# Kernel tuning notes

Measured on AMD Instinct MI355X. Metric: run time of the kernel, lower is better.

Reference implementation:

```python
import jax, jax.numpy as jnp
import numpy as np
from jax import lax

K_NEI = 64      # max_num_neighbors in radius query
NEG = -1e30     # mask value for max-aggregation


def fps(pos, n_sample):
    """Farthest point sampling per cloud. pos: [B,N,3] -> idx [B,n_sample] int32.
    Deterministic start at point 0 (PyG uses a random start)."""
    B, N, _ = pos.shape
    start = jnp.zeros((B,), jnp.int32)
    big = jnp.full((B, N), jnp.finfo(pos.dtype).max, pos.dtype)
    def body(carry, _):
        mind, last = carry
        lp = jnp.take_along_axis(pos, last[:, None, None], axis=1)  # [B,1,3]
        d = jnp.sum((pos - lp) ** 2, -1)                            # [B,N]
        mind = jnp.minimum(mind, d)
        nxt = jnp.argmax(mind, axis=1).astype(jnp.int32)
        return (mind, nxt), nxt
    (_, _), rest = lax.scan(body, (big, start), None, length=n_sample - 1)
    return jnp.concatenate([start[None], rest], 0).T  # [B, n_sample]


def radius_nn(pos_all, pos_q, r, k):
    """Up to k nearest neighbors within radius r (per cloud).
    pos_all: [B,N,3], pos_q: [B,M,3] -> idx [B,M,k] int32, valid [B,M,k] bool."""
    d2 = jnp.sum((pos_q[:, :, None, :] - pos_all[:, None, :, :]) ** 2, -1)  # [B,M,N]
    score = jnp.where(d2 <= r * r, -d2, -jnp.inf)
    vals, idx = lax.top_k(score, k)
    return idx, jnp.isfinite(vals)


def gather(feat, idx):
    """feat: [B,P,C], idx: [B,M,k] -> [B,M,k,C]"""
    B, M, k = idx.shape
    out = jnp.take_along_axis(feat, idx.reshape(B, M * k)[:, :, None], axis=1)
    return out.reshape(B, M, k, feat.shape[-1])


def mlp3(x, w1, b1, w2, b2, w3, b3):
    x = jax.nn.relu(x @ w1 + b1)
    x = jax.nn.relu(x @ w2 + b2)
    return x @ w3 + b3


def point_conv(x, pos_src, pos_dst, nidx, valid, params):
    """PyG PointConv: message = local_nn([x_j, pos_j - pos_i]), max aggregation."""
    rel = gather(pos_src, nidx) - pos_dst[:, :, None, :]          # [B,M,k,3]
    msg = rel if x is None else jnp.concatenate([gather(x, nidx), rel], -1)
    h = mlp3(msg, *params)                                        # [B,M,k,C]
    h = jnp.where(valid[..., None], h, NEG)
    out = jnp.max(h, axis=2)
    return jnp.where(valid.any(2)[..., None], out, 0.0)


def setup_inputs() -> dict:
    key = jax.random.key(0)
    shapes = {
        'sa1_w1': (3, 64), 'sa1_b1': (64,), 'sa1_w2': (64, 64), 'sa1_b2': (64,),
        'sa1_w3': (64, 128), 'sa1_b3': (128,),
        'sa2_w1': (131, 128), 'sa2_b1': (128,), 'sa2_w2': (128, 128), 'sa2_b2': (128,),
        'sa2_w3': (128, 256), 'sa2_b3': (256,),
        'g_w1': (259, 256), 'g_b1': (256,), 'g_w2': (256, 512), 'g_b2': (512,),
        'g_w3': (512, 1024), 'g_b3': (1024,),
        'l1_w': (1024, 512), 'l1_b': (512,), 'l2_w': (512, 256), 'l2_b': (256,),
        'l3_w': (256, 7), 'l3_b': (7,),
    }
    ks = jax.random.split(key, len(shapes) + 1)
    inp = {'points': jax.random.uniform(ks[0], (8, 4096, 3), jnp.float32)}
    for i, (name, shp) in enumerate(shapes.items()):
        inp[name] = jax.random.normal(ks[i + 1], shp, jnp.float32) / np.sqrt(shp[0]).astype(np.float32)
    return inp


def reference(points, sa1_w1, sa1_b1, sa1_w2, sa1_b2, sa1_w3, sa1_b3,
              sa2_w1, sa2_b1, sa2_w2, sa2_b2, sa2_w3, sa2_b3,
              g_w1, g_b1, g_w2, g_b2, g_w3, g_b3,
              l1_w, l1_b, l2_w, l2_b, l3_w, l3_b):
    B, N, _ = points.shape
    pos = points[..., :3]
    # ---- stage 1: fps ratio 0.5, radius 0.1 ----
    N1 = N // 2
    idx1 = fps(pos, N1)
    pos1 = jnp.take_along_axis(pos, idx1[..., None], axis=1)      # [B,N1,3]
    nidx1, valid1 = radius_nn(pos, pos1, 0.1, K_NEI)
    x1 = jax.nn.relu(point_conv(None, pos, pos1, nidx1, valid1,
                                (sa1_w1, sa1_b1, sa1_w2, sa1_b2, sa1_w3, sa1_b3)))
    # ---- stage 2: fps ratio 0.25, radius 0.2 ----
    N2 = N1 // 4
    idx2 = fps(pos1, N2)
    pos2 = jnp.take_along_axis(pos1, idx2[..., None], axis=1)     # [B,N2,3]
    nidx2, valid2 = radius_nn(pos1, pos2, 0.2, K_NEI)
    x2 = jax.nn.relu(point_conv(x1, pos1, pos2, nidx2, valid2,
                                (sa2_w1, sa2_b1, sa2_w2, sa2_b2, sa2_w3, sa2_b3)))
    # ---- global MLP + grouped maxpool over 128 points ----
    g = mlp3(jnp.concatenate([x2, pos2], -1), g_w1, g_b1, g_w2, g_b2, g_w3, g_b3)  # [B,N2,1024]
    g = g.reshape(-1, 128, 1024).max(axis=1)                      # [B*N2/128, 1024]
    h = jax.nn.relu(g @ l1_w + l1_b)                              # dropout = identity (eval)
    h = jax.nn.relu(h @ l2_w + l2_b)
    h = h @ l3_w + l3_b                                           # [B*N2/128, 7]
    b_out = h.reshape(B, -1, 7).mean(axis=1)                      # [B,7]
    t = b_out[:, :3]
    q = b_out[:, 3:]
    q = q / jnp.maximum(jnp.linalg.norm(q, axis=-1, keepdims=True), 1e-12)
    return jnp.concatenate([t, q], axis=-1)
```

## Files before the change

### kernel.cpp

```cpp
#include <hip/hip_runtime.h>
#include <float.h>


typedef float f32x2 __attribute__((ext_vector_type(2)));

__device__ __forceinline__ float d2_rn(float ax, float ay, float az,
                                       float bx, float by, float bz) {
  float dx = __fsub_rn(ax, bx), dy = __fsub_rn(ay, by), dz = __fsub_rn(az, bz);
  return __fadd_rn(__fadd_rn(__fmul_rn(dx, dx), __fmul_rn(dy, dy)), __fmul_rn(dz, dz));
}

template<int CTRL>
__device__ __forceinline__ unsigned long long dppmax(unsigned long long a) {
  const unsigned int lo = (unsigned int)a, hi = (unsigned int)(a >> 32);
  const unsigned int slo =
      (unsigned int)__builtin_amdgcn_update_dpp(0, (int)lo, CTRL, 0xf, 0xf, true);
  const unsigned int shi =
      (unsigned int)__builtin_amdgcn_update_dpp(0, (int)hi, CTRL, 0xf, 0xf, true);
  const unsigned long long s = ((unsigned long long)shi << 32) | slo;
  return s > a ? s : a;
}

__device__ __forceinline__ unsigned int aload(const unsigned int* p) {
  return __hip_atomic_load(p, __ATOMIC_RELAXED, __HIP_MEMORY_SCOPE_AGENT);
}
__device__ __forceinline__ void astore(unsigned int* p, unsigned int v) {
  __hip_atomic_store(p, v, __ATOMIC_RELAXED, __HIP_MEMORY_SCOPE_AGENT);
}

template<int N, int NS, int T>
__device__ __forceinline__ void fps_pub(const float* __restrict__ pb,
                                        float* __restrict__ outp,
                                        unsigned int* __restrict__ pub,
                                        float* sx, float* sy, float* sz,
                                        unsigned long long* s_red) {
  constexpr int P = N / T;
  constexpr int W = T / 64;
  const int t = threadIdx.x;
  for (int i = t; i < N; i += T) { sx[i] = pb[i*3]; sy[i] = pb[i*3+1]; sz[i] = pb[i*3+2]; }
  __syncthreads();
  __builtin_amdgcn_s_setprio(2);
  float px[P], py[P], pz[P], mind[P];
  unsigned int kc[P];
#pragma unroll
  for (int j = 0; j < P; ++j) {
    const int i = j*T + t;
    px[j] = sx[i]; py[j] = sy[i]; pz[j] = sz[i];
    mind[j] = FLT_MAX;
    kc[j] = (unsigned int)(N - 1 - i);
  }
  float lx = sx[0], ly = sy[0], lz = sz[0];
  if (t == 0) {
    astore(&pub[0], 1u);
    outp[0] = lx; outp[1] = ly; outp[2] = lz;
  }
  for (int it = 1; it < NS; ++it) {
    float bv = -1.0f; unsigned int bk = 0;
#pragma unroll
    for (int j = 0; j < P; ++j) {
      const float dx = __fsub_rn(px[j], lx);
      const float dy = __fsub_rn(py[j], ly);
      const float dz = __fsub_rn(pz[j], lz);
      const float d = __fadd_rn(__fadd_rn(__fmul_rn(dx, dx), __fmul_rn(dy, dy)),
                                __fmul_rn(dz, dz));
      const float m = fminf(mind[j], d);
      mind[j] = m;
      const bool gt = m > bv;
      bv = gt ? m : bv;
      bk = gt ? kc[j] : bk;
    }
    unsigned long long key =
        ((unsigned long long)__float_as_uint(bv) << 32) | bk;
    key = dppmax<0x111>(key);
    key = dppmax<0x112>(key);
    key = dppmax<0x114>(key);
    key = dppmax<0x118>(key);
    key = dppmax<0x142>(key);
    key = dppmax<0x143>(key);
    const int par = it & 1;
    if ((t & 63) == 63) s_red[par*W + (t >> 6)] = key;
    __syncthreads();
    unsigned long long best = s_red[par*W];
#pragma unroll
    for (int w = 1; w < W; ++w) {
      const unsigned long long o = s_red[par*W + w];
      best = o > best ? o : best;
    }
    const int idx = (N - 1) - (int)(unsigned int)(best & 0xFFFFFFFFull);
    if (t == 0) astore(&pub[it], (unsigned int)(idx + 1));
    lx = sx[idx]; ly = sy[idx]; lz = sz[idx];
    if (t == 0) {
      outp[(size_t)it*3 + 0] = lx; outp[(size_t)it*3 + 1] = ly; outp[(size_t)it*3 + 2] = lz;
    }
  }
  __builtin_amdgcn_s_setprio(0);
}

struct SmRC1 {
  union { struct { float d2[1024]; int id[1024]; } rad; float x[64 * 64]; } u;
  float rel[64 * 4];
  float out[128];
  int nid[64];
  int qidx;
  int cnt;
};
struct SmRC2 {
  union { struct { float d2[1024]; int id[1024]; } rad; float x[64 * 128]; } u;
  float rel[64 * 4];
  float out[256];
  int nid[64];
  int qidx;
  int cnt;
};

__device__ void rc1_item(int b, int m,
                         const float* __restrict__ points,
                         const unsigned int* __restrict__ sidx1, float r2,
                         const float* __restrict__ w1, const float* __restrict__ b1,
                         const float* __restrict__ w2, const float* __restrict__ b2,
                         const float* __restrict__ w3, const float* __restrict__ b3,
                         float* __restrict__ x1, SmRC1& R) {
  const int t = threadIdx.x;
  const int q = b*2048 + m;
  if (t == 0) {
    unsigned int v;
    while ((v = aload(&sidx1[q])) == 0u) __builtin_amdgcn_s_sleep(16);
    R.qidx = (int)v - 1;
    R.cnt = 0;
  }
  __syncthreads();
  const float* pb = points + (size_t)b * 4096 * 3;
  const int qi = R.qidx;
  const float qx = pb[qi*3], qy = pb[qi*3+1], qz = pb[qi*3+2];
  for (int i = t; i < 4096; i += 256) {
    const float d2 = d2_rn(qx, qy, qz, pb[i*3], pb[i*3+1], pb[i*3+2]);
    if (d2 <= r2) {
      const int p = atomicAdd(&R.cnt, 1);
      if (p < 1024) { R.u.rad.d2[p] = d2; R.u.rad.id[p] = i; }
    }
  }
  __syncthreads();
  const int cntc = min(R.cnt, 1024);
  const int cnt = min(cntc, 64);
  float* outp = x1 + (size_t)q * 128;
  if (cnt == 0) { if (t < 128) outp[t] = 0.f; return; }
  if (cntc <= 64) {
    if (t < cntc) R.nid[t] = R.u.rad.id[t];
  } else {
    for (int c = t; c < cntc; c += 256) {
      const float dc = R.u.rad.d2[c]; const int ic = R.u.rad.id[c];
      int rank = 0;
      for (int jj = 0; jj < cntc; ++jj)
        rank += (R.u.rad.d2[jj] < dc) || (R.u.rad.d2[jj] == dc && R.u.rad.id[jj] < ic);
      if (rank < 64) R.nid[rank] = ic;
    }
  }
  __syncthreads();
  if (t < 64) {
    const int n = (t < cnt) ? R.nid[t] : 0;
    const float* p = points + ((size_t)(b << 12) + n) * 3;
    R.rel[t*4+0] = p[0] - qx; R.rel[t*4+1] = p[1] - qy; R.rel[t*4+2] = p[2] - qz;
  }
  __syncthreads();
  const int j = t & 63;
  const int g = __builtin_amdgcn_readfirstlane(t >> 6);
  float* s_x = R.u.x;
  const int sw  = j & 31;
  const int row = j * 64;
  const float rx = R.rel[j*4+0], ry = R.rel[j*4+1], rz = R.rel[j*4+2];
  f32x2 acc[8];
  { const f32x2* bv = (const f32x2*)(b1 + g*16);
#pragma unroll
    for (int c = 0; c < 8; ++c) acc[c] = bv[c]; }
#pragma unroll
  for (int kk = 0; kk < 3; ++kk) {
    const float xk = (kk == 0) ? rx : ((kk == 1) ? ry : rz);
    const f32x2 xv = {xk, xk};
    const float4* wr = (const float4*)(w1 + kk*64 + g*16);
#pragma unroll
    for (int c4 = 0; c4 < 4; ++c4) {
      const float4 w = wr[c4];
      acc[c4*2+0] += xv * f32x2{w.x, w.y};
      acc[c4*2+1] += xv * f32x2{w.z, w.w};
    }
  }
#pragma unroll
  for (int c = 0; c < 8; ++c) {
    const f32x2 v = acc[c];
    s_x[row + ((g*16 + 2*c + 0) ^ sw)] = fmaxf(v.x, 0.f);
    s_x[row + ((g*16 + 2*c + 1) ^ sw)] = fmaxf(v.y, 0.f);
  }
  __syncthreads();
  { const f32x2* bv = (const f32x2*)(b2 + g*16);
#pragma unroll
    for (int c = 0; c < 8; ++c) acc[c] = bv[c]; }
#pragma unroll 2
  for (int k = 0; k < 64; ++k) {
    const float hk = s_x[row + (k ^ sw)];
    const f32x2 hv = {hk, hk};
    const float4* wr = (const float4*)(w2 + k*64 + g*16);
#pragma unroll
    for (int c4 = 0; c4 < 4; ++c4) {
      const float4 w = wr[c4];
      acc[c4*2+0] += hv * f32x2{w.x, w.y};
      acc[c4*2+1] += hv * f32x2{w.z, w.w};
    }
  }
  __syncthreads();
#pragma unroll
  for (int c = 0; c < 8; ++c) {
    const f32x2 v = acc[c];
    s_x[row + ((g*16 + 2*c + 0) ^ sw)] = fmaxf(v.x, 0.f);
    s_x[row + ((g*16 + 2*c + 1) ^ sw)] = fmaxf(v.y, 0.f);
  }
  __syncthreads();
#pragma unroll 1
  for (int p = 0; p < 2; ++p) {
    f32x2 a[8];
    { const f32x2* bv = (const f32x2*)(b3 + g*32 + p*16);
#pragma unroll
      for (int c = 0; c < 8; ++c) a[c] = bv[c]; }
#pragma unroll 2
    for (int k = 0; k < 64; ++k) {
      const float hk = s_x[row + (k ^ sw)];
      const f32x2 hv = {hk, hk};
      const float4* wr = (const float4*)(w3 + k*128 + g*32 + p*16);
#pragma unroll
      for (int c4 = 0; c4 < 4; ++c4) {
        const float4 w = wr[c4];
        a[c4*2+0] += hv * f32x2{w.x, w.y};
        a[c4*2+1] += hv * f32x2{w.z, w.w};
      }
    }
    if (j >= cnt) {
#pragma unroll
      for (int c = 0; c < 8; ++c) a[c] = f32x2{-1e30f, -1e30f};
    }
#pragma unroll
    for (int off = 32; off > 0; off >>= 1) {
#pragma unroll
      for (int c = 0; c < 8; ++c) {
        a[c].x = fmaxf(a[c].x, __shfl_xor(a[c].x, off, 64));
        a[c].y = fmaxf(a[c].y, __shfl_xor(a[c].y, off, 64));
      }
    }
    if (j == 0) {
#pragma unroll
      for (int c = 0; c < 8; ++c) *(f32x2*)(&R.out[g*32 + p*16 + 2*c]) = a[c];
    }
  }
  __syncthreads();
  if (t < 128) outp[t] = fmaxf(R.out[t], 0.f);
}

__device__ void rc2_item(int b, int m,
                         const float* __restrict__ x1, const float* __restrict__ pos1,
                         const unsigned int* __restrict__ sidx2, float r2,
                         const float* __restrict__ w1, const float* __restrict__ b1,
                         const float* __restrict__ w2, const float* __restrict__ b2,
                         const float* __restrict__ w3, const float* __restrict__ b3,
                         float* __restrict__ x2, SmRC2& R) {
  const int t = threadIdx.x;
  const int q = b*512 + m;
  if (t == 0) {
    unsigned int v;
    while ((v = aload(&sidx2[q])) == 0u) __builtin_amdgcn_s_sleep(16);
    R.qidx = (int)v - 1;
    R.cnt = 0;
  }
  __syncthreads();
  const float* pb = pos1 + (size_t)b * 2048 * 3;
  const int qi = R.qidx;
  const float qx = pb[qi*3], qy = pb[qi*3+1], qz = pb[qi*3+2];
  for (int i = t; i < 2048; i += 256) {
    const float d2 = d2_rn(qx, qy, qz, pb[i*3], pb[i*3+1], pb[i*3+2]);
    if (d2 <= r2) {
      const int p = atomicAdd(&R.cnt, 1);
      if (p < 1024) { R.u.rad.d2[p] = d2; R.u.rad.id[p] = i; }
    }
  }
  __syncthreads();
  const int cntc = min(R.cnt, 1024);
  const int cnt = min(cntc, 64);
  float* outp = x2 + (size_t)q * 256;
  if (cnt == 0) { outp[t] = 0.f; return; }
  if (cntc <= 64) {
    if (t < cntc) R.nid[t] = R.u.rad.id[t];
  } else {
    for (int c = t; c < cntc; c += 256) {
      const float dc = R.u.rad.d2[c]; const int ic = R.u.rad.id[c];
      int rank = 0;
      for (int jj = 0; jj < cntc; ++jj)
        rank += (R.u.rad.d2[jj] < dc) || (R.u.rad.d2[jj] == dc && R.u.rad.id[jj] < ic);
      if (rank < 64) R.nid[rank] = ic;
    }
  }
  __syncthreads();
  if (t < 64) {
    const int n = (t < cnt) ? R.nid[t] : 0;
    const float* p = pos1 + ((size_t)(b << 11) + n) * 3;
    R.rel[t*4+0] = p[0] - qx; R.rel[t*4+1] = p[1] - qy; R.rel[t*4+2] = p[2] - qz;
  }
  __syncthreads();
  float* s_x = R.u.x;
  for (int i = t; i < 64*128; i += 256) {
    const int r = i >> 7, c = i & 127;
    const int n = ((r < cnt) ? R.nid[r] : 0);
    s_x[r*128 + (c ^ (r & 31))] = x1[((size_t)(b << 11) + n)*128 + c];
  }
  __syncthreads();
  const int j = t & 63;
  const int g = __builtin_amdgcn_readfirstlane(t >> 6);
  const int sw  = j & 31;
  const int row = j * 128;
  f32x2 acc[16];
  { const f32x2* bv = (const f32x2*)(b1 + g*32);
#pragma unroll
    for (int c = 0; c < 16; ++c) acc[c] = bv[c]; }
#pragma unroll 2
  for (int k = 0; k < 128; ++k) {
    const float xk = s_x[row + (k ^ sw)];
    const f32x2 xv = {xk, xk};
    const float4* wr = (const float4*)(w1 + k*128 + g*32);
#pragma unroll
    for (int c4 = 0; c4 < 8; ++c4) {
      const float4 w = wr[c4];
      acc[c4*2+0] += xv * f32x2{w.x, w.y};
      acc[c4*2+1] += xv * f32x2{w.z, w.w};
    }
  }
#pragma unroll
  for (int kk = 0; kk < 3; ++kk) {
    const float xk = R.rel[j*4 + kk];
    const f32x2 xv = {xk, xk};
    const float4* wr = (const float4*)(w1 + (128 + kk)*128 + g*32);
#pragma unroll
    for (int c4 = 0; c4 < 8; ++c4) {
      const float4 w = wr[c4];
      acc[c4*2+0] += xv * f32x2{w.x, w.y};
      acc[c4*2+1] += xv * f32x2{w.z, w.w};
    }
  }
  __syncthreads();
#pragma unroll
  for (int c = 0; c < 16; ++c) {
    const f32x2 v = acc[c];
    s_x[row + ((g*32 + 2*c + 0) ^ sw)] = fmaxf(v.x, 0.f);
    s_x[row + ((g*32 + 2*c + 1) ^ sw)] = fmaxf(v.y, 0.f);
  }
  __syncthreads();
  { const f32x2* bv = (const f32x2*)(b2 + g*32);
#pragma unroll
    for (int c = 0; c < 16; ++c) acc[c] = bv[c]; }
#pragma unroll 2
  for (int k = 0; k < 128; ++k) {
    const float hk = s_x[row + (k ^ sw)];
    const f32x2 hv = {hk, hk};
    const float4* wr = (const float4*)(w2 + k*128 + g*32);
#pragma unroll
    for (int c4 = 0; c4 < 8; ++c4) {
      const float4 w = wr[c4];
      acc[c4*2+0] += hv * f32x2{w.x, w.y};
      acc[c4*2+1] += hv * f32x2{w.z, w.w};
    }
  }
  __syncthreads();
#pragma unroll
  for (int c = 0; c < 16; ++c) {
    const f32x2 v = acc[c];
    s_x[row + ((g*32 + 2*c + 0) ^ sw)] = fmaxf(v.x, 0.f);
    s_x[row + ((g*32 + 2*c + 1) ^ sw)] = fmaxf(v.y, 0.f);
  }
  __syncthreads();
#pragma unroll 1
  for (int p = 0; p < 2; ++p) {
    f32x2 a[16];
    { const f32x2* bv = (const f32x2*)(b3 + g*64 + p*32);
#pragma unroll
      for (int c = 0; c < 16; ++c) a[c] = bv[c]; }
#pragma unroll 2
    for (int k = 0; k < 128; ++k) {
      const float hk = s_x[row + (k ^ sw)];
      const f32x2 hv = {hk, hk};
      const float4* wr = (const float4*)(w3 + k*256 + g*64 + p*32);
#pragma unroll
      for (int c4 = 0; c4 < 8; ++c4) {
        const float4 w = wr[c4];
        a[c4*2+0] += hv * f32x2{w.x, w.y};
        a[c4*2+1] += hv * f32x2{w.z, w.w};
      }
    }
    if (j >= cnt) {
#pragma unroll
      for (int c = 0; c < 16; ++c) a[c] = f32x2{-1e30f, -1e30f};
    }
#pragma unroll
    for (int off = 32; off > 0; off >>= 1) {
#pragma unroll
      for (int c = 0; c < 16; ++c) {
        a[c].x = fmaxf(a[c].x, __shfl_xor(a[c].x, off, 64));
        a[c].y = fmaxf(a[c].y, __shfl_xor(a[c].y, off, 64));
      }
    }
    if (j == 0) {
#pragma unroll
      for (int c = 0; c < 16; ++c) *(f32x2*)(&R.out[g*64 + p*32 + 2*c]) = a[c];
    }
  }
  __syncthreads();
  outp[t] = fmaxf(R.out[t], 0.f);
}

struct FpsSm1 { float sx[4096], sy[4096], sz[4096]; unsigned long long red[8]; };
struct FpsSm2 { float sx[2048], sy[2048], sz[2048]; unsigned long long red[8]; };

__global__ __launch_bounds__(256, 3) void mega1_kernel(
    const float* __restrict__ points, float* __restrict__ pos1,
    unsigned int* __restrict__ sidx1, int* __restrict__ qhead, float r2,
    const float* __restrict__ w1, const float* __restrict__ b1,
    const float* __restrict__ w2, const float* __restrict__ b2,
    const float* __restrict__ w3, const float* __restrict__ b3,
    float* __restrict__ x1) {
  __shared__ union U { FpsSm1 f; SmRC1 r; } sm;
  __shared__ int s_item;
  for (;;) {
    __syncthreads();
    if (threadIdx.x == 0) s_item = atomicAdd(qhead, 1);
    __syncthreads();
    const int w = s_item;
    if (w >= 8 + 8*2048) return;
    if (w < 8) {
      fps_pub<4096, 2048, 256>(points + (size_t)w*4096*3, pos1 + (size_t)w*2048*3,
                               sidx1 + w*2048, sm.f.sx, sm.f.sy, sm.f.sz, sm.f.red);
    } else {
      const int qq = w - 8;
      rc1_item(qq & 7, qq >> 3, points, sidx1, r2, w1, b1, w2, b2, w3, b3, x1, sm.r);
    }
  }
}

__global__ __launch_bounds__(256, 4) void mega2_kernel(
    const float* __restrict__ x1, const float* __restrict__ pos1,
    float* __restrict__ pos2,
    unsigned int* __restrict__ sidx2, int* __restrict__ qhead, float r2,
    const float* __restrict__ w1, const float* __restrict__ b1,
    const float* __restrict__ w2, const float* __restrict__ b2,
    const float* __restrict__ w3, const float* __restrict__ b3,
    float* __restrict__ x2) {
  __shared__ union U { FpsSm2 f; SmRC2 r; } sm;
  __shared__ int s_item;
  for (;;) {
    __syncthreads();
    if (threadIdx.x == 0) s_item = atomicAdd(qhead, 1);
    __syncthreads();
    const int w = s_item;
    if (w >= 8 + 8*512) return;
    if (w < 8) {
      fps_pub<2048, 512, 256>(pos1 + (size_t)w*2048*3, pos2 + (size_t)w*512*3,
                              sidx2 + w*512, sm.f.sx, sm.f.sy, sm.f.sz, sm.f.red);
    } else {
      const int qq = w - 8;
      rc2_item(qq & 7, qq >> 3, x1, pos1, sidx2, r2, w1, b1, w2, b2, w3, b3, x2, sm.r);
    }
  }
}

__global__ __launch_bounds__(256) void gmlp_kernel(
    const float* __restrict__ x2, const float* __restrict__ pos2,
    const float* __restrict__ w1, const float* __restrict__ b1,
    const float* __restrict__ w2, const float* __restrict__ b2,
    const float* __restrict__ w3, const float* __restrict__ b3,
    float* __restrict__ gpart) {
  const int blk = blockIdx.x;
  const int t = threadIdx.x;
  __shared__ float sA[260 * 18];
  __shared__ float sB[512 * 18];
  const int p0 = blk * 16;
  for (int i = t; i < 16*256; i += 256) {
    const int p = i >> 8, k = i & 255;
    sA[k*18 + p] = x2[(size_t)(p0 + p)*256 + k];
  }
  if (t < 48) { const int p = t/3, c = t%3; sA[(256+c)*18 + p] = pos2[(size_t)(p0+p)*3 + c]; }
  __syncthreads();
  f32x2 h1[8];
  { const float bb = b1[t];
#pragma unroll
    for (int p8 = 0; p8 < 8; ++p8) h1[p8] = f32x2{bb, bb}; }
#pragma unroll 2
  for (int k = 0; k < 259; ++k) {
    const float w = w1[(size_t)k*256 + t];
    const f32x2 wv = {w, w};
    const f32x2* row = (const f32x2*)(&sA[k*18]);
#pragma unroll
    for (int p8 = 0; p8 < 8; ++p8) h1[p8] += row[p8] * wv;
  }
  __syncthreads();
#pragma unroll
  for (int p8 = 0; p8 < 8; ++p8) {
    f32x2 a = h1[p8];
    a.x = fmaxf(a.x, 0.f); a.y = fmaxf(a.y, 0.f);
    *(f32x2*)(&sA[t*18 + 2*p8]) = a;
  }
  __syncthreads();
  f32x2 h2a[8], h2b[8];
  { const float ba = b2[t], bb = b2[t + 256];
#pragma unroll
    for (int p8 = 0; p8 < 8; ++p8) { h2a[p8] = f32x2{ba, ba}; h2b[p8] = f32x2{bb, bb}; } }
#pragma unroll 2
  for (int k = 0; k < 256; ++k) {
    const float wa = w2[(size_t)k*512 + t];
    const float wb = w2[(size_t)k*512 + t + 256];
    const f32x2 wav = {wa, wa}, wbv = {wb, wb};
    const f32x2* row = (const f32x2*)(&sA[k*18]);
#pragma unroll
    for (int p8 = 0; p8 < 8; ++p8) { const f32x2 x = row[p8]; h2a[p8] += x*wav; h2b[p8] += x*wbv; }
  }
  __syncthreads();
#pragma unroll
  for (int p8 = 0; p8 < 8; ++p8) {
    f32x2 a = h2a[p8], c = h2b[p8];
    a.x = fmaxf(a.x, 0.f); a.y = fmaxf(a.y, 0.f);
    c.x = fmaxf(c.x, 0.f); c.y = fmaxf(c.y, 0.f);
    *(f32x2*)(&sB[t*18 + 2*p8]) = a;
    *(f32x2*)(&sB[(t+256)*18 + 2*p8]) = c;
  }
  __syncthreads();
  f32x2 a3[4][8];
#pragma unroll
  for (int c = 0; c < 4; ++c) {
    const float bb = b3[t + c*256];
#pragma unroll
    for (int p8 = 0; p8 < 8; ++p8) a3[c][p8] = f32x2{bb, bb};
  }
#pragma unroll 2
  for (int k = 0; k < 512; ++k) {
    const f32x2* row = (const f32x2*)(&sB[k*18]);
    f32x2 xk[8];
#pragma unroll
    for (int p8 = 0; p8 < 8; ++p8) xk[p8] = row[p8];
#pragma unroll
    for (int c = 0; c < 4; ++c) {
      const float w = w3[(size_t)k*1024 + t + c*256];
      const f32x2 wv = {w, w};
#pragma unroll
      for (int p8 = 0; p8 < 8; ++p8) a3[c][p8] += xk[p8] * wv;
    }
  }
#pragma unroll
  for (int c = 0; c < 4; ++c) {
    f32x2 m2 = a3[c][0];
#pragma unroll
    for (int p8 = 1; p8 < 8; ++p8) {
      m2.x = fmaxf(m2.x, a3[c][p8].x); m2.y = fmaxf(m2.y, a3[c][p8].y);
    }
    gpart[(size_t)blk*1024 + t + c*256] = fmaxf(m2.x, m2.y);
  }
}

__global__ __launch_bounds__(256) void head_kernel(
    const float* __restrict__ gpart,
    const float* __restrict__ l1w, const float* __restrict__ l1b,
    const float* __restrict__ l2w, const float* __restrict__ l2b,
    const float* __restrict__ l3w, const float* __restrict__ l3b,
    float* __restrict__ h3) {
  const int r = blockIdx.x, t = threadIdx.x;
  __shared__ float sIn[1024];
  __shared__ float sH[512];
  __shared__ float sH2[256];
  for (int i = t; i < 1024; i += 256) {
    float v = gpart[(size_t)(r*8)*1024 + i];
#pragma unroll
    for (int rr = 1; rr < 8; ++rr) v = fmaxf(v, gpart[(size_t)(r*8 + rr)*1024 + i]);
    sIn[i] = v;
  }
  __syncthreads();
  float a0 = l1b[t], a1 = l1b[t + 256];
#pragma unroll 4
  for (int k = 0; k < 1024; ++k) {
    const float x = sIn[k];
    a0 += x * l1w[(size_t)k*512 + t];
    a1 += x * l1w[(size_t)k*512 + t + 256];
  }
  sH[t] = fmaxf(a0, 0.f); sH[t+256] = fmaxf(a1, 0.f);
  __syncthreads();
  float a = l2b[t];
#pragma unroll 4
  for (int k = 0; k < 512; ++k) a += sH[k] * l2w[(size_t)k*256 + t];
  sH2[t] = fmaxf(a, 0.f);
  __syncthreads();
  if (t < 7) {
    float acc = l3b[t];
#pragma unroll 4
    for (int k = 0; k < 256; ++k) acc += sH2[k] * l3w[(size_t)k*7 + t];
    h3[(size_t)r*7 + t] = acc;
  }
}

__global__ void final_kernel(const float* __restrict__ h3, float* __restrict__ out) {
  const int b = threadIdx.x;
  if (b >= 8) return;
  float v[7];
#pragma unroll
  for (int c = 0; c < 7; ++c) {
    const float s = ((h3[(b*4+0)*7+c] + h3[(b*4+1)*7+c]) + h3[(b*4+2)*7+c]) + h3[(b*4+3)*7+c];
    v[c] = s * 0.25f;
  }
  const float nrm = fmaxf(sqrtf(((v[3]*v[3] + v[4]*v[4]) + v[5]*v[5]) + v[6]*v[6]), 1e-12f);
  out[b*7+0] = v[0]; out[b*7+1] = v[1]; out[b*7+2] = v[2];
  out[b*7+3] = v[3]/nrm; out[b*7+4] = v[4]/nrm;
  out[b*7+5] = v[5]/nrm; out[b*7+6] = v[6]/nrm;
}

extern "C" void kernel_launch(void* const* d_in, const int* in_sizes, int n_in,
                              void* d_out, int out_size, void* d_ws, size_t ws_size,
                              hipStream_t stream) {
  const float* points = (const float*)d_in[0];
  const float* sa1_w1 = (const float*)d_in[1];
  const float* sa1_b1 = (const float*)d_in[2];
  const float* sa1_w2 = (const float*)d_in[3];
  const float* sa1_b2 = (const float*)d_in[4];
  const float* sa1_w3 = (const float*)d_in[5];
  const float* sa1_b3 = (const float*)d_in[6];
  const float* sa2_w1 = (const float*)d_in[7];
  const float* sa2_b1 = (const float*)d_in[8];
  const float* sa2_w2 = (const float*)d_in[9];
  const float* sa2_b2 = (const float*)d_in[10];
  const float* sa2_w3 = (const float*)d_in[11];
  const float* sa2_b3 = (const float*)d_in[12];
  const float* g_w1   = (const float*)d_in[13];
  const float* g_b1   = (const float*)d_in[14];
  const float* g_w2   = (const float*)d_in[15];
  const float* g_b2   = (const float*)d_in[16];
  const float* g_w3   = (const float*)d_in[17];
  const float* g_b3   = (const float*)d_in[18];
  const float* l1_w   = (const float*)d_in[19];
  const float* l1_b   = (const float*)d_in[20];
  const float* l2_w   = (const float*)d_in[21];
  const float* l2_b   = (const float*)d_in[22];
  const float* l3_w   = (const float*)d_in[23];
  const float* l3_b   = (const float*)d_in[24];

  unsigned int* u = (unsigned int*)d_ws;
  unsigned int* sidx1 = u;
  unsigned int* sidx2 = u + 16384;
  int* qhead1 = (int*)(u + 16384 + 4096);
  int* qhead2 = qhead1 + 1;
  const size_t syncWords = 16384 + 4096 + 2;

  float* ws = (float*)d_ws + 20608;
  size_t o = 0;
  float* pos1  = ws + o; o += (size_t)8*2048*3;
  float* pos2  = ws + o; o += (size_t)8*512*3;
  float* x1    = ws + o; o += (size_t)8*2048*128;
  float* x2    = ws + o; o += (size_t)8*512*256;
  float* gpart = ws + o; o += (size_t)256*1024;
  float* h3    = ws + o; o += (size_t)32*7;

  hipMemsetAsync(d_ws, 0, syncWords * 4, stream);

  const float R2_1 = (float)(0.1 * 0.1);
  const float R2_2 = (float)(0.2 * 0.2);

  mega1_kernel<<<768, 256, 0, stream>>>(points, pos1, sidx1, qhead1, R2_1,
                                        sa1_w1, sa1_b1, sa1_w2, sa1_b2, sa1_w3, sa1_b3, x1);
  mega2_kernel<<<1024, 256, 0, stream>>>(x1, pos1, pos2, sidx2, qhead2, R2_2,
                                         sa2_w1, sa2_b1, sa2_w2, sa2_b2, sa2_w3, sa2_b3, x2);
  gmlp_kernel<<<256, 256, 0, stream>>>(x2, pos2, g_w1, g_b1, g_w2, g_b2, g_w3, g_b3, gpart);
  head_kernel<<<32, 256, 0, stream>>>(gpart, l1_w, l1_b, l2_w, l2_b, l3_w, l3_b, h3);
  final_kernel<<<1, 64, 0, stream>>>(h3, (float*)d_out);
}
```

Baseline: 2.390 ms.

## Run stage-2 FPS inside stage-1 megakernel, streaming from stage-1 FPS output

Stage-2 farthest point sampling now runs as extra work items in the first persistent kernel. It pulls each stage-1 sampled index as soon as it is published, so the stage-2 FPS chain overlaps the stage-1 FPS and grouping work instead of waiting for a second kernel launch. The radius-conv of stage 2 becomes an ordinary one-block-per-query kernel. The FPS inner loop is also rewritten to process two points per lane with packed float2 math, and the reduction barrier becomes a raw lgkmcnt wait plus s_barrier. The risks are that the stage-2 FPS blocks spin while occupying slots in the first kernel, and that the packed path could change how the floating-point expressions are fused.

```diff
diff --git a/kernel.cpp b/kernel.cpp
--- a/kernel.cpp
+++ b/kernel.cpp
@@ -28,26 +28,32 @@
   __hip_atomic_store(p, v, __ATOMIC_RELAXED, __HIP_MEMORY_SCOPE_AGENT);
 }
 
+__device__ __forceinline__ void barrier_lgkm() {
+  asm volatile("s_waitcnt lgkmcnt(0)\n\ts_barrier" ::: "memory");
+}
+
 template<int N, int NS, int T>
-__device__ __forceinline__ void fps_pub(const float* __restrict__ pb,
-                                        float* __restrict__ outp,
-                                        unsigned int* __restrict__ pub,
-                                        float* sx, float* sy, float* sz,
-                                        unsigned long long* s_red) {
+__device__ void fps_core(float* sx, float* sy, float* sz,
+                         unsigned long long* s_red,
+                         float* __restrict__ outp,
+                         unsigned int* __restrict__ pub) {
+#pragma clang fp contract(off)
   constexpr int P = N / T;
+  constexpr int P2 = P / 2;
   constexpr int W = T / 64;
   const int t = threadIdx.x;
-  for (int i = t; i < N; i += T) { sx[i] = pb[i*3]; sy[i] = pb[i*3+1]; sz[i] = pb[i*3+2]; }
-  __syncthreads();
   __builtin_amdgcn_s_setprio(2);
-  float px[P], py[P], pz[P], mind[P];
-  unsigned int kc[P];
-#pragma unroll
-  for (int j = 0; j < P; ++j) {
-    const int i = j*T + t;
-    px[j] = sx[i]; py[j] = sy[i]; pz[j] = sz[i];
-    mind[j] = FLT_MAX;
-    kc[j] = (unsigned int)(N - 1 - i);
+  f32x2 px[P2], py[P2], pz[P2], mind[P2];
+  unsigned int kc0[P2], kc1[P2];
+#pragma unroll
+  for (int j = 0; j < P2; ++j) {
+    const int i0 = (2*j)*T + t, i1 = i0 + T;
+    px[j] = f32x2{sx[i0], sx[i1]};
+    py[j] = f32x2{sy[i0], sy[i1]};
+    pz[j] = f32x2{sz[i0], sz[i1]};
+    mind[j] = f32x2{FLT_MAX, FLT_MAX};
+    kc0[j] = (unsigned int)(N - 1 - i0);
+    kc1[j] = (unsigned int)(N - 1 - i1);
   }
   float lx = sx[0], ly = sy[0], lz = sz[0];
   if (t == 0) {
@@ -55,22 +61,26 @@
     outp[0] = lx; outp[1] = ly; outp[2] = lz;
   }
   for (int it = 1; it < NS; ++it) {
-    float bv = -1.0f; unsigned int bk = 0;
-#pragma unroll
-    for (int j = 0; j < P; ++j) {
-      const float dx = __fsub_rn(px[j], lx);
-      const float dy = __fsub_rn(py[j], ly);
-      const float dz = __fsub_rn(pz[j], lz);
-      const float d = __fadd_rn(__fadd_rn(__fmul_rn(dx, dx), __fmul_rn(dy, dy)),
-                                __fmul_rn(dz, dz));
-      const float m = fminf(mind[j], d);
-      mind[j] = m;
-      const bool gt = m > bv;
-      bv = gt ? m : bv;
-      bk = gt ? kc[j] : bk;
-    }
-    unsigned long long key =
-        ((unsigned long long)__float_as_uint(bv) << 32) | bk;
+    const f32x2 lx2 = {lx, lx}, ly2 = {ly, ly}, lz2 = {lz, lz};
+    float bv0 = -1.0f, bv1 = -1.0f;
+    unsigned int bk0 = 0, bk1 = 0;
+#pragma unroll
+    for (int j = 0; j < P2; ++j) {
+      const f32x2 dx = px[j] - lx2;
+      const f32x2 dy = py[j] - ly2;
+      const f32x2 dz = pz[j] - lz2;
+      const f32x2 s = ((dx*dx) + (dy*dy)) + (dz*dz);
+      const float m0 = fminf(mind[j].x, s.x);
+      const float m1 = fminf(mind[j].y, s.y);
+      mind[j] = f32x2{m0, m1};
+      const bool g0 = m0 > bv0;
+      bv0 = g0 ? m0 : bv0; bk0 = g0 ? kc0[j] : bk0;
+      const bool g1 = m1 > bv1;
+      bv1 = g1 ? m1 : bv1; bk1 = g1 ? kc1[j] : bk1;
+    }
+    const unsigned long long k0 = ((unsigned long long)__float_as_uint(bv0) << 32) | bk0;
+    const unsigned long long k1 = ((unsigned long long)__float_as_uint(bv1) << 32) | bk1;
+    unsigned long long key = k0 > k1 ? k0 : k1;
     key = dppmax<0x111>(key);
     key = dppmax<0x112>(key);
     key = dppmax<0x114>(key);
@@ -79,7 +89,7 @@
     key = dppmax<0x143>(key);
     const int par = it & 1;
     if ((t & 63) == 63) s_red[par*W + (t >> 6)] = key;
-    __syncthreads();
+    barrier_lgkm();
     unsigned long long best = s_red[par*W];
 #pragma unroll
     for (int w = 1; w < W; ++w) {
@@ -96,6 +106,7 @@
   __builtin_amdgcn_s_setprio(0);
 }
 
+struct FpsSm { float sx[4096], sy[4096], sz[4096]; unsigned long long red[8]; };
 struct SmRC1 {
   union { struct { float d2[1024]; int id[1024]; } rad; float x[64 * 64]; } u;
   float rel[64 * 4];
@@ -253,15 +264,62 @@
   if (t < 128) outp[t] = fmaxf(R.out[t], 0.f);
 }
 
-__device__ void rc2_item(int b, int m,
-                         const float* __restrict__ x1, const float* __restrict__ pos1,
-                         const unsigned int* __restrict__ sidx2, float r2,
-                         const float* __restrict__ w1, const float* __restrict__ b1,
-                         const float* __restrict__ w2, const float* __restrict__ b2,
-                         const float* __restrict__ w3, const float* __restrict__ b3,
-                         float* __restrict__ x2, SmRC2& R) {
+__global__ __launch_bounds__(256, 3) void mega1_kernel(
+    const float* __restrict__ points, float* __restrict__ pos1,
+    float* __restrict__ pos2,
+    unsigned int* __restrict__ sidx1, unsigned int* __restrict__ sidx2,
+    int* __restrict__ qhead, float r2,
+    const float* __restrict__ w1, const float* __restrict__ b1,
+    const float* __restrict__ w2, const float* __restrict__ b2,
+    const float* __restrict__ w3, const float* __restrict__ b3,
+    float* __restrict__ x1) {
+  __shared__ union U { FpsSm f; SmRC1 r; } sm;
+  __shared__ int s_item;
   const int t = threadIdx.x;
-  const int q = b*512 + m;
+  for (;;) {
+    __syncthreads();
+    if (t == 0) s_item = atomicAdd(qhead, 1);
+    __syncthreads();
+    const int w = s_item;
+    if (w >= 16 + 8*2048) return;
+    if (w < 8) {
+      const float* pb = points + (size_t)w * 4096 * 3;
+      for (int i = t; i < 4096; i += 256) {
+        sm.f.sx[i] = pb[i*3]; sm.f.sy[i] = pb[i*3+1]; sm.f.sz[i] = pb[i*3+2];
+      }
+      __syncthreads();
+      fps_core<4096, 2048, 256>(sm.f.sx, sm.f.sy, sm.f.sz, sm.f.red,
+                                pos1 + (size_t)w*2048*3, sidx1 + w*2048);
+    } else if (w < 16) {
+      const int b = w - 8;
+      const float* pb = points + (size_t)b * 4096 * 3;
+      for (int i = t; i < 2048; i += 256) {
+        unsigned int v;
+        while ((v = aload(&sidx1[b*2048 + i])) == 0u) __builtin_amdgcn_s_sleep(16);
+        const int idx = (int)v - 1;
+        sm.f.sx[i] = pb[idx*3]; sm.f.sy[i] = pb[idx*3+1]; sm.f.sz[i] = pb[idx*3+2];
+      }
+      __syncthreads();
+      fps_core<2048, 512, 256>(sm.f.sx, sm.f.sy, sm.f.sz, sm.f.red,
+                               pos2 + (size_t)b*512*3, sidx2 + b*512);
+    } else {
+      const int qq = w - 16;
+      rc1_item(qq & 7, qq >> 3, points, sidx1, r2, w1, b1, w2, b2, w3, b3, x1, sm.r);
+    }
+  }
+}
+
+__global__ __launch_bounds__(256, 4) void rc2_kernel(
+    const float* __restrict__ x1, const float* __restrict__ pos1,
+    const unsigned int* __restrict__ sidx2, float r2,
+    const float* __restrict__ w1, const float* __restrict__ b1,
+    const float* __restrict__ w2, const float* __restrict__ b2,
+    const float* __restrict__ w3, const float* __restrict__ b3,
+    float* __restrict__ x2) {
+  __shared__ SmRC2 R;
+  const int q = blockIdx.x;
+  const int b = q >> 9;
+  const int t = threadIdx.x;
   if (t == 0) {
     unsigned int v;
     while ((v = aload(&sidx2[q])) == 0u) __builtin_amdgcn_s_sleep(16);
@@ -409,60 +467,6 @@
   }
   __syncthreads();
   outp[t] = fmaxf(R.out[t], 0.f);
-}
-
-struct FpsSm1 { float sx[4096], sy[4096], sz[4096]; unsigned long long red[8]; };
-struct FpsSm2 { float sx[2048], sy[2048], sz[2048]; unsigned long long red[8]; };
-
-__global__ __launch_bounds__(256, 3) void mega1_kernel(
-    const float* __restrict__ points, float* __restrict__ pos1,
-    unsigned int* __restrict__ sidx1, int* __restrict__ qhead, float r2,
-    const float* __restrict__ w1, const float* __restrict__ b1,
-    const float* __restrict__ w2, const float* __restrict__ b2,
-    const float* __restrict__ w3, const float* __restrict__ b3,
-    float* __restrict__ x1) {
-  __shared__ union U { FpsSm1 f; SmRC1 r; } sm;
-  __shared__ int s_item;
-  for (;;) {
-    __syncthreads();
-    if (threadIdx.x == 0) s_item = atomicAdd(qhead, 1);
-    __syncthreads();
-    const int w = s_item;
-    if (w >= 8 + 8*2048) return;
-    if (w < 8) {
-      fps_pub<4096, 2048, 256>(points + (size_t)w*4096*3, pos1 + (size_t)w*2048*3,
-                               sidx1 + w*2048, sm.f.sx, sm.f.sy, sm.f.sz, sm.f.red);
-    } else {
-      const int qq = w - 8;
-      rc1_item(qq & 7, qq >> 3, points, sidx1, r2, w1, b1, w2, b2, w3, b3, x1, sm.r);
-    }
-  }
-}
-
-__global__ __launch_bounds__(256, 4) void mega2_kernel(
-    const float* __restrict__ x1, const float* __restrict__ pos1,
-    float* __restrict__ pos2,
-    unsigned int* __restrict__ sidx2, int* __restrict__ qhead, float r2,
-    const float* __restrict__ w1, const float* __restrict__ b1,
-    const float* __restrict__ w2, const float* __restrict__ b2,
-    const float* __restrict__ w3, const float* __restrict__ b3,
-    float* __restrict__ x2) {
-  __shared__ union U { FpsSm2 f; SmRC2 r; } sm;
-  __shared__ int s_item;
-  for (;;) {
-    __syncthreads();
-    if (threadIdx.x == 0) s_item = atomicAdd(qhead, 1);
-    __syncthreads();
-    const int w = s_item;
-    if (w >= 8 + 8*512) return;
-    if (w < 8) {
-      fps_pub<2048, 512, 256>(pos1 + (size_t)w*2048*3, pos2 + (size_t)w*512*3,
-                              sidx2 + w*512, sm.f.sx, sm.f.sy, sm.f.sz, sm.f.red);
-    } else {
-      const int qq = w - 8;
-      rc2_item(qq & 7, qq >> 3, x1, pos1, sidx2, r2, w1, b1, w2, b2, w3, b3, x2, sm.r);
-    }
-  }
 }
 
 __global__ __launch_bounds__(256) void gmlp_kernel(
@@ -644,8 +648,7 @@
   unsigned int* sidx1 = u;
   unsigned int* sidx2 = u + 16384;
   int* qhead1 = (int*)(u + 16384 + 4096);
-  int* qhead2 = qhead1 + 1;
-  const size_t syncWords = 16384 + 4096 + 2;
+  const size_t syncWords = 16384 + 4096 + 1;
 
   float* ws = (float*)d_ws + 20608;
   size_t o = 0;
@@ -661,10 +664,10 @@
   const float R2_1 = (float)(0.1 * 0.1);
   const float R2_2 = (float)(0.2 * 0.2);
 
-  mega1_kernel<<<768, 256, 0, stream>>>(points, pos1, sidx1, qhead1, R2_1,
+  mega1_kernel<<<768, 256, 0, stream>>>(points, pos1, pos2, sidx1, sidx2, qhead1, R2_1,
                                         sa1_w1, sa1_b1, sa1_w2, sa1_b2, sa1_w3, sa1_b3, x1);
-  mega2_kernel<<<1024, 256, 0, stream>>>(x1, pos1, pos2, sidx2, qhead2, R2_2,
-                                         sa2_w1, sa2_b1, sa2_w2, sa2_b2, sa2_w3, sa2_b3, x2);
+  rc2_kernel<<<8*512, 256, 0, stream>>>(x1, pos1, sidx2, R2_2,
+                                        sa2_w1, sa2_b1, sa2_w2, sa2_b2, sa2_w3, sa2_b3, x2);
   gmlp_kernel<<<256, 256, 0, stream>>>(x2, pos2, g_w1, g_b1, g_w2, g_b2, g_w3, g_b3, gpart);
   head_kernel<<<32, 256, 0, stream>>>(gpart, l1_w, l1_b, l2_w, l2_b, l3_w, l3_b, h3);
   final_kernel<<<1, 64, 0, stream>>>(h3, (float*)d_out);
```

Result: no change. 2.387 ms (-0.1%).
